# Optimization experiments

Hardware: AMD Instinct MI355X
Metric: run time of the kernel (lower is better)

Reference implementation:

```python
import jax, jax.numpy as jnp
import numpy as np

N = 8192      # number of nodes; input feature dim == N (identity-style features)
HID = 200     # hidden dim hard-coded in GCNConv(adj.shape[0], 200)
OUT = 5       # out_dim (sentiment classes)


def setup_inputs() -> dict:
    key = jax.random.key(0)
    k1, k2, k3, k4 = jax.random.split(key, 4)
    x = jax.random.normal(k1, (N, N), dtype=jnp.float32)
    adj = jax.random.uniform(k2, (N, N), dtype=jnp.float32)
    W1 = jax.random.normal(k3, (N, HID), dtype=jnp.float32) * (1.0 / np.sqrt(N))
    b1 = jnp.zeros((HID,), dtype=jnp.float32)
    W2 = jax.random.normal(k4, (HID, OUT), dtype=jnp.float32) * (1.0 / np.sqrt(HID))
    b2 = jnp.zeros((OUT,), dtype=jnp.float32)
    return {"x": x, "adj": adj, "W1": W1, "b1": b1, "W2": W2, "b2": b2}


def gcn_conv(adj, x, W, b):
    # support = X @ W (cheap, small output dim), then propagate: adj @ support
    return adj @ (x @ W) + b


def reference(x, adj, W1, b1, W2, b2):
    h = jax.nn.relu(gcn_conv(adj, x, W1, b1))      # [N, 200]
    logits = gcn_conv(adj, h, W2, b2)              # [N, 5]
    return jax.nn.softmax(logits, axis=-1)
```

## Files before the change

### kernel.cpp

```cpp
#include <hip/hip_runtime.h>
#include <hip/hip_fp16.h>
#include <math.h>

#define NN   8192
#define KD   8192
#define HID  200
#define NP   224
#define OUTC 5

#define BM   128
#define BK   64
#define KS   8
#define KCH  (KD / KS)
#define NT   (KCH / BK)
#define TUB  1792
#define BFSZ (NP * BK)

typedef _Float16 f16;
typedef __attribute__((ext_vector_type(4))) _Float16 f16x4;
typedef __attribute__((ext_vector_type(8))) _Float16 f16x8;
typedef __attribute__((ext_vector_type(4))) float f32x4;

__device__ __forceinline__ void fill16(const f16* g, f16* l) {
    __builtin_amdgcn_global_load_lds(
        (const __attribute__((address_space(1))) void*)g,
        (__attribute__((address_space(3))) void*)l, 16, 0, 0);
}

__global__ __launch_bounds__(256) void k_prep_w1(const float* __restrict__ W1,
                                                 f16* __restrict__ Bsw) {
    __shared__ float tile[64][65];
    const int kt = blockIdx.x;
    const int n0 = blockIdx.y * 64;
    const int k0 = kt * 64;
    const int t = threadIdx.x;
    #pragma unroll
    for (int q = 0; q < 4; ++q) {
        int idx4 = t + q * 256;
        int kk = idx4 >> 4, nn4 = (idx4 & 15) * 4;
        int n = n0 + nn4;
        float4 v = {0.f, 0.f, 0.f, 0.f};
        if (n + 4 <= HID) v = *(const float4*)(W1 + (size_t)(k0 + kk) * HID + n);
        tile[kk][nn4 + 0] = v.x; tile[kk][nn4 + 1] = v.y;
        tile[kk][nn4 + 2] = v.z; tile[kk][nn4 + 3] = v.w;
    }
    __syncthreads();
    #pragma unroll
    for (int p2 = 0; p2 < 2; ++p2) {
        int u = t + p2 * 256;
        int rl = u >> 3, cphys = u & 7;
        int r = n0 + rl;
        if (r < NP) {
            int ck = cphys ^ (r & 7);
            f16x8 o;
            #pragma unroll
            for (int h = 0; h < 8; ++h) o[h] = (f16)tile[ck * 8 + h][rl];
            *(f16x8*)(Bsw + ((size_t)kt * TUB + r * 8 + cphys) * 8) = o;
        }
    }
}

__global__ __launch_bounds__(512, 4) void k_gemm(const float* __restrict__ A,
                                                 const f16* __restrict__ Bsw,
                                                 f16* __restrict__ CP) {
    __shared__ __align__(16) f16 Ah[BM * BK];
    __shared__ __align__(16) f16 Bf[2 * BFSZ];

    const int t = threadIdx.x;
    const int lane = t & 63, wv = t >> 6;
    const int wm = wv >> 1, wn = wv & 1;
    const int l15 = lane & 15, g = lane >> 4;
    const int bid = blockIdx.x;
    const int ky = bid & 7;
    const int bx = bid >> 3;
    const int m0 = bx * BM;
    const int kt0 = ky * NT;
    const size_t kc0 = (size_t)ky * KCH;

    const int ar = t >> 2;
    const int ac = (t & 3) * 2;
    const int swzA = ar & 7;
    f16* aw0 = &Ah[(ar * 8 + ((ac + 0) ^ swzA)) * 8];
    f16* aw1 = &Ah[(ar * 8 + ((ac + 1) ^ swzA)) * 8];
    const float* ap = A + (size_t)(m0 + ar) * KD + kc0 + (size_t)(t & 3) * 16;

    const f16* bsrc = Bsw + ((size_t)kt0 * TUB + (size_t)(wv * 64 + lane)) * 8;

    f32x4 acc[2][7];
    #pragma unroll
    for (int m = 0; m < 2; ++m)
        #pragma unroll
        for (int n = 0; n < 7; ++n) acc[m][n] = (f32x4){0.f, 0.f, 0.f, 0.f};

    float4 v0, v1, v2, v3;
#define LOADA(i) { const float* p_ = ap + (size_t)(i) * BK;            \
        v0 = *(const float4*)(p_);      v1 = *(const float4*)(p_ + 4);  \
        v2 = *(const float4*)(p_ + 8);  v3 = *(const float4*)(p_ + 12); }
#define FILLB(i, b) {                                                   \
        const f16* bs_ = bsrc + (size_t)(i) * (TUB * 8);                \
        f16* bd_ = &Bf[(size_t)(b) * BFSZ];                             \
        fill16(bs_,            bd_ + (0    + wv * 64) * 8);             \
        fill16(bs_ + 512 * 8,  bd_ + (512  + wv * 64) * 8);             \
        fill16(bs_ + 1024 * 8, bd_ + (1024 + wv * 64) * 8);             \
        if (wv < 4) fill16(bs_ + 1536 * 8, bd_ + (1536 + wv * 64) * 8); \
    }

    FILLB(0, 0);
    LOADA(0);
    for (int i = 0; i < NT; ++i) {
        if (i + 1 < NT) FILLB(i + 1, (i + 1) & 1);
        {
            f16x8 h0, h1;
            h0[0]=(f16)v0.x; h0[1]=(f16)v0.y; h0[2]=(f16)v0.z; h0[3]=(f16)v0.w;
            h0[4]=(f16)v1.x; h0[5]=(f16)v1.y; h0[6]=(f16)v1.z; h0[7]=(f16)v1.w;
            h1[0]=(f16)v2.x; h1[1]=(f16)v2.y; h1[2]=(f16)v2.z; h1[3]=(f16)v2.w;
            h1[4]=(f16)v3.x; h1[5]=(f16)v3.y; h1[6]=(f16)v3.z; h1[7]=(f16)v3.w;
            *(f16x8*)aw0 = h0;
            *(f16x8*)aw1 = h1;
        }
        if (i + 1 < NT) LOADA(i + 1);
        asm volatile("s_waitcnt lgkmcnt(0)\n\ts_barrier" ::: "memory");

        const f16* bb = &Bf[(size_t)(i & 1) * BFSZ];
        __builtin_amdgcn_s_setprio(1);
        #pragma unroll
        for (int kk = 0; kk < 2; ++kk) {
            const int cu = kk * 4 + g;
            f16x8 a0, a1;
            { int r = wm * 32 + l15;      a0 = *(const f16x8*)&Ah[(r * 8 + (cu ^ (r & 7))) * 8]; }
            { int r = wm * 32 + 16 + l15; a1 = *(const f16x8*)&Ah[(r * 8 + (cu ^ (r & 7))) * 8]; }
            #pragma unroll
            for (int n = 0; n < 7; ++n) {
                int cr = wn * 112 + n * 16 + l15;
                f16x8 b = *(const f16x8*)&bb[(cr * 8 + (cu ^ (cr & 7))) * 8];
                acc[0][n] = __builtin_amdgcn_mfma_f32_16x16x32_f16(a0, b, acc[0][n], 0, 0, 0);
                acc[1][n] = __builtin_amdgcn_mfma_f32_16x16x32_f16(a1, b, acc[1][n], 0, 0, 0);
            }
        }
        __builtin_amdgcn_s_setprio(0);
        asm volatile("s_barrier" ::: "memory");
    }
#undef LOADA
#undef FILLB

    f16* o = CP + (size_t)ky * ((size_t)NN * NP);
    #pragma unroll
    for (int m = 0; m < 2; ++m) {
        #pragma unroll
        for (int n = 0; n < 7; ++n) {
            int rb = m0 + wm * 32 + m * 16 + g * 4;
            int c = wn * 112 + n * 16 + l15;
            #pragma unroll
            for (int r = 0; r < 4; ++r)
                o[(size_t)(rb + r) * NP + c] = (f16)acc[m][n][r];
        }
    }
}

__global__ __launch_bounds__(256) void k_combine_b(const f16* __restrict__ CP,
                                                   f16* __restrict__ Bsw) {
    __shared__ float tile[64][65];
    const size_t SZ = (size_t)NN * NP;
    const int kt = blockIdx.x;
    const int n0 = blockIdx.y * 64;
    const int k0 = kt * 64;
    const int t = threadIdx.x;
    #pragma unroll
    for (int q = 0; q < 4; ++q) {
        int idx4 = t + q * 256;
        int kk = idx4 >> 4, nn4 = (idx4 & 15) * 4;
        int n = n0 + nn4;
        float s0 = 0.f, s1 = 0.f, s2 = 0.f, s3 = 0.f;
        if (n < NP) {
            #pragma unroll
            for (int p = 0; p < KS; ++p) {
                f16x4 v = *(const f16x4*)(CP + (size_t)p * SZ + (size_t)(k0 + kk) * NP + n);
                s0 += (float)v[0]; s1 += (float)v[1]; s2 += (float)v[2]; s3 += (float)v[3];
            }
        }
        tile[kk][nn4 + 0] = s0; tile[kk][nn4 + 1] = s1;
        tile[kk][nn4 + 2] = s2; tile[kk][nn4 + 3] = s3;
    }
    __syncthreads();
    #pragma unroll
    for (int p2 = 0; p2 < 2; ++p2) {
        int u = t + p2 * 256;
        int rl = u >> 3, cphys = u & 7;
        int r = n0 + rl;
        if (r < NP) {
            int ck = cphys ^ (r & 7);
            f16x8 o;
            #pragma unroll
            for (int h = 0; h < 8; ++h) o[h] = (f16)tile[ck * 8 + h][rl];
            *(f16x8*)(Bsw + ((size_t)kt * TUB + r * 8 + cphys) * 8) = o;
        }
    }
}

__global__ __launch_bounds__(256) void k_tail(const f16* __restrict__ CP,
                                              const float* __restrict__ b1,
                                              const float* __restrict__ W2,
                                              float* __restrict__ S2T) {
    const int tx = threadIdx.x;
    const int ty = threadIdx.y;
    const int row = blockIdx.x * 8 + ty;
    float s[OUTC] = {0.f, 0.f, 0.f, 0.f, 0.f};
    if (tx < 28) {
        const size_t SZ = (size_t)NN * NP;
        const size_t off = (size_t)row * NP + tx * 8;
        float h[8] = {0.f,0.f,0.f,0.f,0.f,0.f,0.f,0.f};
        #pragma unroll
        for (int p = 0; p < KS; ++p) {
            f16x8 v = *(const f16x8*)(CP + (size_t)p * SZ + off);
            #pragma unroll
            for (int j = 0; j < 8; ++j) h[j] += (float)v[j];
        }
        #pragma unroll
        for (int j = 0; j < 8; ++j) {
            int c = tx * 8 + j;
            if (c < HID) {
                float hv = fmaxf(h[j] + b1[c], 0.f);
                #pragma unroll
                for (int q = 0; q < OUTC; ++q) s[q] += hv * W2[c * OUTC + q];
            }
        }
    }
    #pragma unroll
    for (int q = 0; q < OUTC; ++q)
        #pragma unroll
        for (int off2 = 16; off2; off2 >>= 1) s[q] += __shfl_down(s[q], off2, 32);
    if (tx == 0) {
        #pragma unroll
        for (int q = 0; q < OUTC; ++q) S2T[(size_t)q * NN + row] = s[q];
    }
}

__global__ __launch_bounds__(256) void k_final(const float* __restrict__ adj,
                                               const float* __restrict__ S2T,
                                               const float* __restrict__ b2,
                                               float* __restrict__ out) {
    __shared__ float red[4][8][OUTC];
    const int t = threadIdx.x, wave = t >> 6, lane = t & 63;
    const int row0 = blockIdx.x * 8;
    float acc[8][OUTC];
    #pragma unroll
    for (int r = 0; r < 8; ++r)
        #pragma unroll
        for (int c = 0; c < OUTC; ++c) acc[r][c] = 0.f;

    for (int jj = 0; jj < 8; ++jj) {
        int kb = (t + jj * 256) * 4;
        float4 s2[OUTC];
        #pragma unroll
        for (int c = 0; c < OUTC; ++c) s2[c] = *(const float4*)(S2T + (size_t)c * NN + kb);
        #pragma unroll
        for (int r = 0; r < 8; ++r) {
            float4 a = *(const float4*)(adj + (size_t)(row0 + r) * KD + kb);
            #pragma unroll
            for (int c = 0; c < OUTC; ++c)
                acc[r][c] += a.x * s2[c].x + a.y * s2[c].y + a.z * s2[c].z + a.w * s2[c].w;
        }
    }
    #pragma unroll
    for (int r = 0; r < 8; ++r)
        #pragma unroll
        for (int c = 0; c < OUTC; ++c) {
            float v = acc[r][c];
            #pragma unroll
            for (int off = 32; off; off >>= 1) v += __shfl_down(v, off, 64);
            if (lane == 0) red[wave][r][c] = v;
        }
    __syncthreads();
    if (t < 8) {
        int r = t;
        float lg[OUTC];
        #pragma unroll
        for (int c = 0; c < OUTC; ++c)
            lg[c] = red[0][r][c] + red[1][r][c] + red[2][r][c] + red[3][r][c] + b2[c];
        float mx = lg[0];
        #pragma unroll
        for (int c = 1; c < OUTC; ++c) mx = fmaxf(mx, lg[c]);
        float e[OUTC], ssum = 0.f;
        #pragma unroll
        for (int c = 0; c < OUTC; ++c) { e[c] = expf(lg[c] - mx); ssum += e[c]; }
        float inv = 1.0f / ssum;
        #pragma unroll
        for (int c = 0; c < OUTC; ++c) out[(size_t)(row0 + r) * OUTC + c] = e[c] * inv;
    }
}

extern "C" void kernel_launch(void* const* d_in, const int* in_sizes, int n_in,
                              void* d_out, int out_size, void* d_ws, size_t ws_size,
                              hipStream_t stream) {
    const float* x   = (const float*)d_in[0];
    const float* adj = (const float*)d_in[1];
    const float* W1  = (const float*)d_in[2];
    const float* b1  = (const float*)d_in[3];
    const float* W2  = (const float*)d_in[4];
    const float* b2  = (const float*)d_in[5];
    float* out = (float*)d_out;

    char* ws = (char*)d_ws;
    const size_t BSZ = (size_t)NP * KD * sizeof(f16);
    f16*   BW1 = (f16*)(ws);
    f16*   BS1 = (f16*)(ws + BSZ);
    float* S2T = (float*)(ws + 2 * BSZ);
    f16*   CP  = (f16*)(ws + 2 * BSZ + 256 * 1024);

    k_prep_w1<<<dim3(128, 4), 256, 0, stream>>>(W1, BW1);
    k_gemm<<<dim3(512), 512, 0, stream>>>(x, BW1, CP);
    k_combine_b<<<dim3(128, 4), 256, 0, stream>>>(CP, BS1);
    k_gemm<<<dim3(512), 512, 0, stream>>>(adj, BS1, CP);
    k_tail<<<dim3(NN / 8), dim3(32, 8), 0, stream>>>(CP, b1, W2, S2T);
    k_final<<<dim3(NN / 8), 256, 0, stream>>>(adj, S2T, b2, out);
}
```

Baseline: 245.9 us.

## Halve GEMM K-tile and double-buffer A and B with one barrier per step

```diff
diff --git a/kernel.cpp b/kernel.cpp
--- a/kernel.cpp
+++ b/kernel.cpp
@@ -9,18 +9,21 @@
 #define OUTC 5
 
 #define BM   128
-#define BK   64
+#define BK   32
 #define KS   8
 #define KCH  (KD / KS)
 #define NT   (KCH / BK)
-#define TUB  1792
-#define BFSZ (NP * BK)
+#define TUB  896
 
 typedef _Float16 f16;
 typedef __attribute__((ext_vector_type(4))) _Float16 f16x4;
 typedef __attribute__((ext_vector_type(8))) _Float16 f16x8;
 typedef __attribute__((ext_vector_type(4))) float f32x4;
 
+__device__ __forceinline__ int swzu(int r, int c) {
+    return (r * 4 + (c ^ (r & 3))) ^ (r & 4);
+}
+
 __device__ __forceinline__ void fill16(const f16* g, f16* l) {
     __builtin_amdgcn_global_load_lds(
         (const __attribute__((address_space(1))) void*)g,
@@ -30,9 +33,9 @@
 __global__ __launch_bounds__(256) void k_prep_w1(const float* __restrict__ W1,
                                                  f16* __restrict__ Bsw) {
     __shared__ float tile[64][65];
-    const int kt = blockIdx.x;
+    const int bx = blockIdx.x;
     const int n0 = blockIdx.y * 64;
-    const int k0 = kt * 64;
+    const int k0 = bx * 64;
     const int t = threadIdx.x;
     #pragma unroll
     for (int q = 0; q < 4; ++q) {
@@ -48,14 +51,14 @@
     #pragma unroll
     for (int p2 = 0; p2 < 2; ++p2) {
         int u = t + p2 * 256;
-        int rl = u >> 3, cphys = u & 7;
+        int rl = u >> 3, cc = u & 7;
+        int ktl = cc >> 2, c = cc & 3;
         int r = n0 + rl;
         if (r < NP) {
-            int ck = cphys ^ (r & 7);
             f16x8 o;
             #pragma unroll
-            for (int h = 0; h < 8; ++h) o[h] = (f16)tile[ck * 8 + h][rl];
-            *(f16x8*)(Bsw + ((size_t)kt * TUB + r * 8 + cphys) * 8) = o;
+            for (int h = 0; h < 8; ++h) o[h] = (f16)tile[ktl * 32 + c * 8 + h][rl];
+            *(f16x8*)(Bsw + ((size_t)(bx * 2 + ktl) * TUB + swzu(r, c)) * 8) = o;
         }
     }
 }
@@ -63,8 +66,8 @@
 __global__ __launch_bounds__(512, 4) void k_gemm(const float* __restrict__ A,
                                                  const f16* __restrict__ Bsw,
                                                  f16* __restrict__ CP) {
-    __shared__ __align__(16) f16 Ah[BM * BK];
-    __shared__ __align__(16) f16 Bf[2 * BFSZ];
+    __shared__ __align__(16) f16 Af0[BM * BK], Af1[BM * BK];
+    __shared__ __align__(16) f16 Bf0[NP * BK], Bf1[NP * BK];
 
     const int t = threadIdx.x;
     const int lane = t & 63, wv = t >> 6;
@@ -77,71 +80,73 @@
     const int kt0 = ky * NT;
     const size_t kc0 = (size_t)ky * KCH;
 
-    const int ar = t >> 2;
-    const int ac = (t & 3) * 2;
-    const int swzA = ar & 7;
-    f16* aw0 = &Ah[(ar * 8 + ((ac + 0) ^ swzA)) * 8];
-    f16* aw1 = &Ah[(ar * 8 + ((ac + 1) ^ swzA)) * 8];
-    const float* ap = A + (size_t)(m0 + ar) * KD + kc0 + (size_t)(t & 3) * 16;
-
+    const int ar = t >> 2, aq = t & 3;
+    const int au = swzu(ar, aq) * 8;
+    const float* ap = A + (size_t)(m0 + ar) * KD + kc0 + (size_t)aq * 8;
     const f16* bsrc = Bsw + ((size_t)kt0 * TUB + (size_t)(wv * 64 + lane)) * 8;
 
+    const int a0o = swzu(wm * 32 + l15, g) * 8;
+    const int bo0 = swzu(wn * 112 + l15, g) * 8;
+
     f32x4 acc[2][7];
     #pragma unroll
     for (int m = 0; m < 2; ++m)
         #pragma unroll
         for (int n = 0; n < 7; ++n) acc[m][n] = (f32x4){0.f, 0.f, 0.f, 0.f};
 
-    float4 v0, v1, v2, v3;
-#define LOADA(i) { const float* p_ = ap + (size_t)(i) * BK;            \
-        v0 = *(const float4*)(p_);      v1 = *(const float4*)(p_ + 4);  \
-        v2 = *(const float4*)(p_ + 8);  v3 = *(const float4*)(p_ + 12); }
-#define FILLB(i, b) {                                                   \
-        const f16* bs_ = bsrc + (size_t)(i) * (TUB * 8);                \
-        f16* bd_ = &Bf[(size_t)(b) * BFSZ];                             \
-        fill16(bs_,            bd_ + (0    + wv * 64) * 8);             \
-        fill16(bs_ + 512 * 8,  bd_ + (512  + wv * 64) * 8);             \
-        fill16(bs_ + 1024 * 8, bd_ + (1024 + wv * 64) * 8);             \
-        if (wv < 4) fill16(bs_ + 1536 * 8, bd_ + (1536 + wv * 64) * 8); \
-    }
-
-    FILLB(0, 0);
-    LOADA(0);
-    for (int i = 0; i < NT; ++i) {
-        if (i + 1 < NT) FILLB(i + 1, (i + 1) & 1);
-        {
-            f16x8 h0, h1;
-            h0[0]=(f16)v0.x; h0[1]=(f16)v0.y; h0[2]=(f16)v0.z; h0[3]=(f16)v0.w;
-            h0[4]=(f16)v1.x; h0[5]=(f16)v1.y; h0[6]=(f16)v1.z; h0[7]=(f16)v1.w;
-            h1[0]=(f16)v2.x; h1[1]=(f16)v2.y; h1[2]=(f16)v2.z; h1[3]=(f16)v2.w;
-            h1[4]=(f16)v3.x; h1[5]=(f16)v3.y; h1[6]=(f16)v3.z; h1[7]=(f16)v3.w;
-            *(f16x8*)aw0 = h0;
-            *(f16x8*)aw1 = h1;
-        }
-        if (i + 1 < NT) LOADA(i + 1);
-        asm volatile("s_waitcnt lgkmcnt(0)\n\ts_barrier" ::: "memory");
-
-        const f16* bb = &Bf[(size_t)(i & 1) * BFSZ];
+    float4 va0, va1, vb0, vb1;
+#define LOADA(i, V0, V1) { const float* p_ = ap + (size_t)(i) * BK;  \
+        V0 = *(const float4*)p_; V1 = *(const float4*)(p_ + 4); }
+#define CONV_STORE(AF, V0, V1) { f16x8 hh_;                                   \
+        hh_[0]=(f16)V0.x; hh_[1]=(f16)V0.y; hh_[2]=(f16)V0.z; hh_[3]=(f16)V0.w; \
+        hh_[4]=(f16)V1.x; hh_[5]=(f16)V1.y; hh_[6]=(f16)V1.z; hh_[7]=(f16)V1.w; \
+        *(f16x8*)&AF[au] = hh_; }
+#define FILLB(i, BF) { const f16* bs_ = bsrc + (size_t)(i) * (TUB * 8);  \
+        fill16(bs_, &BF[(wv * 64) * 8]);                                 \
+        if (wv < 6) fill16(bs_ + 512 * 8, &BF[(512 + wv * 64) * 8]); }
+#define MFMA_PH(AF, BF) {                                                \
+        f16x8 a0_ = *(const f16x8*)&AF[a0o];                             \
+        f16x8 a1_ = *(const f16x8*)&AF[a0o + 512];                       \
+        _Pragma("unroll")                                                \
+        for (int n = 0; n < 7; ++n) {                                    \
+            f16x8 b_ = *(const f16x8*)&BF[bo0 + n * 512];                \
+            acc[0][n] = __builtin_amdgcn_mfma_f32_16x16x32_f16(a0_, b_, acc[0][n], 0, 0, 0); \
+            acc[1][n] = __builtin_amdgcn_mfma_f32_16x16x32_f16(a1_, b_, acc[1][n], 0, 0, 0); } }
+
+    LOADA(0, va0, va1); LOADA(1, vb0, vb1);
+    FILLB(0, Bf0);
+    CONV_STORE(Af0, va0, va1);
+    asm volatile("s_waitcnt vmcnt(0) lgkmcnt(0)\n\ts_barrier" ::: "memory");
+
+    #pragma unroll 1
+    for (int ip = 0; ip < NT / 2 - 1; ++ip) {
+        const int i = 2 * ip;
+        FILLB(i + 1, Bf1);
+        CONV_STORE(Af1, vb0, vb1);
+        LOADA(i + 2, va0, va1);
         __builtin_amdgcn_s_setprio(1);
-        #pragma unroll
-        for (int kk = 0; kk < 2; ++kk) {
-            const int cu = kk * 4 + g;
-            f16x8 a0, a1;
-            { int r = wm * 32 + l15;      a0 = *(const f16x8*)&Ah[(r * 8 + (cu ^ (r & 7))) * 8]; }
-            { int r = wm * 32 + 16 + l15; a1 = *(const f16x8*)&Ah[(r * 8 + (cu ^ (r & 7))) * 8]; }
-            #pragma unroll
-            for (int n = 0; n < 7; ++n) {
-                int cr = wn * 112 + n * 16 + l15;
-                f16x8 b = *(const f16x8*)&bb[(cr * 8 + (cu ^ (cr & 7))) * 8];
-                acc[0][n] = __builtin_amdgcn_mfma_f32_16x16x32_f16(a0, b, acc[0][n], 0, 0, 0);
-                acc[1][n] = __builtin_amdgcn_mfma_f32_16x16x32_f16(a1, b, acc[1][n], 0, 0, 0);
-            }
-        }
+        MFMA_PH(Af0, Bf0);
         __builtin_amdgcn_s_setprio(0);
-        asm volatile("s_barrier" ::: "memory");
-    }
+        asm volatile("s_waitcnt vmcnt(2) lgkmcnt(0)\n\ts_barrier" ::: "memory");
+        FILLB(i + 2, Bf0);
+        CONV_STORE(Af0, va0, va1);
+        LOADA(i + 3, vb0, vb1);
+        __builtin_amdgcn_s_setprio(1);
+        MFMA_PH(Af1, Bf1);
+        __builtin_amdgcn_s_setprio(0);
+        asm volatile("s_waitcnt vmcnt(2) lgkmcnt(0)\n\ts_barrier" ::: "memory");
+    }
+    FILLB(NT - 1, Bf1);
+    CONV_STORE(Af1, vb0, vb1);
+    __builtin_amdgcn_s_setprio(1);
+    MFMA_PH(Af0, Bf0);
+    __builtin_amdgcn_s_setprio(0);
+    asm volatile("s_waitcnt vmcnt(0) lgkmcnt(0)\n\ts_barrier" ::: "memory");
+    MFMA_PH(Af1, Bf1);
 #undef LOADA
+#undef CONV_STORE
 #undef FILLB
+#undef MFMA_PH
 
     f16* o = CP + (size_t)ky * ((size_t)NN * NP);
     #pragma unroll
@@ -161,9 +166,9 @@
                                                    f16* __restrict__ Bsw) {
     __shared__ float tile[64][65];
     const size_t SZ = (size_t)NN * NP;
-    const int kt = blockIdx.x;
+    const int bx = blockIdx.x;
     const int n0 = blockIdx.y * 64;
-    const int k0 = kt * 64;
+    const int k0 = bx * 64;
     const int t = threadIdx.x;
     #pragma unroll
     for (int q = 0; q < 4; ++q) {
@@ -185,14 +190,14 @@
     #pragma unroll
     for (int p2 = 0; p2 < 2; ++p2) {
         int u = t + p2 * 256;
-        int rl = u >> 3, cphys = u & 7;
+        int rl = u >> 3, cc = u & 7;
+        int ktl = cc >> 2, c = cc & 3;
         int r = n0 + rl;
         if (r < NP) {
-            int ck = cphys ^ (r & 7);
             f16x8 o;
             #pragma unroll
-            for (int h = 0; h < 8; ++h) o[h] = (f16)tile[ck * 8 + h][rl];
-            *(f16x8*)(Bsw + ((size_t)kt * TUB + r * 8 + cphys) * 8) = o;
+            for (int h = 0; h < 8; ++h) o[h] = (f16)tile[ktl * 32 + c * 8 + h][rl];
+            *(f16x8*)(Bsw + ((size_t)(bx * 2 + ktl) * TUB + swzu(r, c)) * 8) = o;
         }
     }
 }
```

Result: slower. 252.6 us (+2.7%).
